# Kernel optimization log

Hardware: AMD Instinct MI355X
Metric: run time of the kernel (lower is better)

The kernel has to match this reference:

```python
import jax, jax.numpy as jnp
import numpy as np
import math

D_MODEL = 1024
H = 16
D_K = D_MODEL // H
D_FF = 4096
NEG = -1e9


def layer_norm(x, alpha, bias):
    # Faithful to source: mean over last dim, UNBIASED std (torch.std default),
    # eps defined in source but never used in forward.
    mean = jnp.mean(x, axis=-1, keepdims=True)
    std = jnp.std(x, axis=-1, ddof=1, keepdims=True)
    return (x - mean) / std * alpha + bias


def mha(x, mask, w_q, w_k, w_v, w_o):
    B, S, D = x.shape
    q = (x @ w_q.T).reshape(B, S, H, D_K)
    k = (x @ w_k.T).reshape(B, S, H, D_K)
    v = (x @ w_v.T).reshape(B, S, H, D_K)
    scores = jnp.einsum('bqhd,bkhd->bhqk', q, k) / math.sqrt(D_K)
    scores = jnp.where(mask, NEG, scores)
    attn = jax.nn.softmax(scores, axis=-1)
    out = jnp.einsum('bhqk,bkhd->bqhd', attn, v).reshape(B, S, D)
    return out @ w_o.T


def setup_inputs() -> dict:
    key = jax.random.key(0)
    ks = jax.random.split(key, 16)
    B, S = 4, 2048
    s = 0.02
    return {
        'x': jax.random.normal(ks[0], (B, S, D_MODEL), jnp.float32),
        'w_q': jax.random.normal(ks[1], (D_MODEL, D_MODEL), jnp.float32) * s,
        'w_k': jax.random.normal(ks[2], (D_MODEL, D_MODEL), jnp.float32) * s,
        'w_v': jax.random.normal(ks[3], (D_MODEL, D_MODEL), jnp.float32) * s,
        'w_o': jax.random.normal(ks[4], (D_MODEL, D_MODEL), jnp.float32) * s,
        'l1_w': jax.random.normal(ks[5], (D_FF, D_MODEL), jnp.float32) * s,
        'l1_b': jnp.zeros((D_FF,), jnp.float32),
        'l2_w': jax.random.normal(ks[6], (D_MODEL, D_FF), jnp.float32) * s,
        'l2_b': jnp.zeros((D_MODEL,), jnp.float32),
        'norm1_a': jnp.ones((D_MODEL,), jnp.float32),
        'norm1_b': jnp.zeros((D_MODEL,), jnp.float32),
        'norm2_a': jnp.ones((D_MODEL,), jnp.float32),
        'norm2_b': jnp.zeros((D_MODEL,), jnp.float32),
        'normf_a': jnp.ones((D_MODEL,), jnp.float32),
        'normf_b': jnp.zeros((D_MODEL,), jnp.float32),
        'mask': jax.random.randint(ks[7], (B, 1, 1, S), 0, 2) == 1,
    }


def reference(x, w_q, w_k, w_v, w_o, l1_w, l1_b, l2_w, l2_b,
              norm1_a, norm1_b, norm2_a, norm2_b, normf_a, normf_b, mask):
    # residual 1: pre-norm self-attention (dropout is identity at eval)
    x = x + mha(layer_norm(x, norm1_a, norm1_b), mask, w_q, w_k, w_v, w_o)
    # residual 2: pre-norm FFN
    h = layer_norm(x, norm2_a, norm2_b)
    ff = jax.nn.relu(h @ l1_w.T + l1_b) @ l2_w.T + l2_b
    x = x + ff
    return layer_norm(x, normf_a, normf_b)
```

## Files before the change

kernel.cpp:

```cpp
#include <hip/hip_runtime.h>
#include <hip/hip_bf16.h>


typedef __bf16 bf16x8 __attribute__((ext_vector_type(8)));
typedef float f32x4 __attribute__((ext_vector_type(4)));
typedef unsigned short u16x8 __attribute__((ext_vector_type(8)));
using bf16 = __hip_bfloat16;

__device__ __forceinline__ f32x4 mfma16(bf16x8 a, bf16x8 b, f32x4 c) {
  return __builtin_amdgcn_mfma_f32_16x16x32_bf16(a, b, c, 0, 0, 0);
}

__device__ __forceinline__ int swz(int row, int blk) {
  return row * 64 + ((blk ^ (row & 7)) << 3);
}

__device__ __forceinline__ void stage_tile64(unsigned short* lds,
                                             const bf16* g, int ld, int rows) {
  const int lane = threadIdx.x & 63, wid = threadIdx.x >> 6;
  const int r8 = lane >> 3, blk = lane & 7;
  const bf16* gl = g + (size_t)r8 * ld + ((blk ^ r8) << 3);
  const int passes = rows >> 3;
  for (int p = wid; p < passes; p += 4) {
    __builtin_amdgcn_global_load_lds(
        (const __attribute__((address_space(1))) void*)(gl + (size_t)(p * 8) * ld),
        (__attribute__((address_space(3))) void*)(lds + p * 512),
        16, 0, 0);
  }
}

__device__ __forceinline__ short bfb(float x) {
  return (short)__hip_bfloat16_raw(__float2bfloat16(x)).x;
}

__global__ __launch_bounds__(256) void cvt_k(const float* __restrict__ s,
                                             bf16* __restrict__ d, int n) {
  const int i = (blockIdx.x * 256 + threadIdx.x) * 4;
  if (i + 3 < n) {
    const float4 v = *reinterpret_cast<const float4*>(s + i);
    ushort4 o;
    o.x = (unsigned short)bfb(v.x);
    o.y = (unsigned short)bfb(v.y);
    o.z = (unsigned short)bfb(v.z);
    o.w = (unsigned short)bfb(v.w);
    *reinterpret_cast<ushort4*>(d + i) = o;
  }
}

template <bool OUT_F32>
__global__ __launch_bounds__(256) void layernorm_k(const float* __restrict__ in,
                                                   const float* __restrict__ gamma,
                                                   const float* __restrict__ beta,
                                                   void* __restrict__ out) {
  __shared__ float red[8];
  const int row = blockIdx.x, t = threadIdx.x;
  const float4 vv = reinterpret_cast<const float4*>(in + (size_t)row * 1024)[t];
  const float x0 = vv.x, x1 = vv.y, x2 = vv.z, x3 = vv.w;
  float s = x0 + x1 + x2 + x3;
#pragma unroll
  for (int off = 32; off; off >>= 1) s += __shfl_down(s, off);
  if ((t & 63) == 0) red[t >> 6] = s;
  __syncthreads();
  const float mean = (red[0] + red[1] + red[2] + red[3]) * (1.0f / 1024.0f);
  const float d0 = x0 - mean, d1 = x1 - mean, d2 = x2 - mean, d3 = x3 - mean;
  float sq = d0 * d0 + d1 * d1 + d2 * d2 + d3 * d3;
#pragma unroll
  for (int off = 32; off; off >>= 1) sq += __shfl_down(sq, off);
  if ((t & 63) == 0) red[4 + (t >> 6)] = sq;
  __syncthreads();
  const float var =
      fmaxf((red[4] + red[5] + red[6] + red[7]) * (1.0f / 1023.0f), 1e-20f);
  const float rstd = rsqrtf(var);
  const float4 ga = reinterpret_cast<const float4*>(gamma)[t];
  const float4 be = reinterpret_cast<const float4*>(beta)[t];
  const float y0 = d0 * rstd * ga.x + be.x;
  const float y1 = d1 * rstd * ga.y + be.y;
  const float y2 = d2 * rstd * ga.z + be.z;
  const float y3 = d3 * rstd * ga.w + be.w;
  if (OUT_F32) {
    reinterpret_cast<float4*>((float*)out + (size_t)row * 1024)[t] =
        make_float4(y0, y1, y2, y3);
  } else {
    ushort4 o;
    o.x = (unsigned short)bfb(y0);
    o.y = (unsigned short)bfb(y1);
    o.z = (unsigned short)bfb(y2);
    o.w = (unsigned short)bfb(y3);
    reinterpret_cast<ushort4*>((bf16*)out + (size_t)row * 1024)[t] = o;
  }
}

template <bool HAS_BIAS, bool RELU, bool HAS_RES, bool OUT_F32>
__global__ __launch_bounds__(256) void gemm_bt(const bf16* __restrict__ A,
                                               const bf16* __restrict__ W,
                                               const float* __restrict__ bias,
                                               const float* __restrict__ resid,
                                               void* __restrict__ out,
                                               int M, int N, int K,
                                               int lda, int ldw) {
  __shared__ __align__(16) unsigned short As[128 * 64];
  __shared__ __align__(16) unsigned short Bs[128 * 64];
  const int lane = threadIdx.x & 63, wid = threadIdx.x >> 6;
  const int n16 = lane & 15, quad = lane >> 4;
  const int wm = (wid >> 1) * 64, wn = (wid & 1) * 64;
  const int tm = blockIdx.x * 128, tn = blockIdx.y * 128;
  f32x4 acc[4][4] = {};
  for (int k0 = 0; k0 < K; k0 += 64) {
    stage_tile64(As, A + (size_t)tm * lda + k0, lda, 128);
    stage_tile64(Bs, W + (size_t)tn * ldw + k0, ldw, 128);
    __syncthreads();
#pragma unroll
    for (int kk = 0; kk < 64; kk += 32) {
      bf16x8 af[4], bw[4];
#pragma unroll
      for (int i = 0; i < 4; ++i)
        af[i] = *reinterpret_cast<const bf16x8*>(
            &As[swz(wm + i * 16 + n16, (kk >> 3) + quad)]);
#pragma unroll
      for (int j = 0; j < 4; ++j)
        bw[j] = *reinterpret_cast<const bf16x8*>(
            &Bs[swz(wn + j * 16 + n16, (kk >> 3) + quad)]);
#pragma unroll
      for (int i = 0; i < 4; ++i)
#pragma unroll
        for (int j = 0; j < 4; ++j) acc[i][j] = mfma16(af[i], bw[j], acc[i][j]);
    }
    __syncthreads();
  }
#pragma unroll
  for (int i = 0; i < 4; ++i) {
#pragma unroll
    for (int j = 0; j < 4; ++j) {
      const int n = tn + wn + j * 16 + n16;
      const float bv = HAS_BIAS ? bias[n] : 0.0f;
#pragma unroll
      for (int r = 0; r < 4; ++r) {
        const int m = tm + wm + i * 16 + quad * 4 + r;
        float vv = acc[i][j][r] + bv;
        if (RELU) vv = fmaxf(vv, 0.0f);
        if (HAS_RES) vv += resid[(size_t)m * N + n];
        if (OUT_F32)
          ((float*)out)[(size_t)m * N + n] = vv;
        else
          ((bf16*)out)[(size_t)m * N + n] = __float2bfloat16(vv);
      }
    }
  }
}

__global__ __launch_bounds__(256) void gemm_qkv_k(const bf16* __restrict__ ln1,
                                                  const bf16* __restrict__ cln,
                                                  const bf16* __restrict__ wqkv,
                                                  const int* __restrict__ cnt,
                                                  bf16* __restrict__ qout,
                                                  bf16* __restrict__ kvout) {
  __shared__ __align__(16) unsigned short As[128 * 64];
  __shared__ __align__(16) unsigned short Bs[128 * 64];
  const int tm = blockIdx.x * 128, by = blockIdx.y;
  const bool isQ = (by < 8);
  if (!isQ) {
    const int npad = (cnt[tm >> 11] + 127) & ~127;
    if ((tm & 2047) >= npad) return;
  }
  const bf16* Ap = isQ ? ln1 : cln;
  const int tn = by * 128;
  const int lane = threadIdx.x & 63, wid = threadIdx.x >> 6;
  const int n16 = lane & 15, quad = lane >> 4;
  const int wm = (wid >> 1) * 64, wn = (wid & 1) * 64;
  f32x4 acc[4][4] = {};
  for (int k0 = 0; k0 < 1024; k0 += 64) {
    stage_tile64(As, Ap + (size_t)tm * 1024 + k0, 1024, 128);
    stage_tile64(Bs, wqkv + (size_t)tn * 1024 + k0, 1024, 128);
    __syncthreads();
#pragma unroll
    for (int kk = 0; kk < 64; kk += 32) {
      bf16x8 af[4], bw[4];
#pragma unroll
      for (int i = 0; i < 4; ++i)
        af[i] = *reinterpret_cast<const bf16x8*>(
            &As[swz(wm + i * 16 + n16, (kk >> 3) + quad)]);
#pragma unroll
      for (int j = 0; j < 4; ++j)
        bw[j] = *reinterpret_cast<const bf16x8*>(
            &Bs[swz(wn + j * 16 + n16, (kk >> 3) + quad)]);
#pragma unroll
      for (int i = 0; i < 4; ++i)
#pragma unroll
        for (int j = 0; j < 4; ++j) acc[i][j] = mfma16(af[i], bw[j], acc[i][j]);
    }
    __syncthreads();
  }
  bf16* outp = isQ ? qout : kvout;
  const int ldo = isQ ? 1024 : 2048;
  const int nc0 = isQ ? tn : tn - 1024;
#pragma unroll
  for (int i = 0; i < 4; ++i) {
#pragma unroll
    for (int j = 0; j < 4; ++j) {
      const int n = nc0 + wn + j * 16 + n16;
#pragma unroll
      for (int r = 0; r < 4; ++r) {
        const int m = tm + wm + i * 16 + quad * 4 + r;
        outp[(size_t)m * ldo + n] = __float2bfloat16(acc[i][j][r]);
      }
    }
  }
}

__global__ __launch_bounds__(256) void prep_mask_k(const int* __restrict__ m,
                                                   float* __restrict__ mf,
                                                   int n) {
  __shared__ int s;
  if (threadIdx.x == 0) s = 0;
  __syncthreads();
  unsigned int acc = 0;
  for (int i = threadIdx.x; i < 512; i += 256)
    acc |= ((const unsigned int*)m)[i] & 0xFFFFFF00u;
  if (acc) atomicOr(&s, 1);
  __syncthreads();
  const bool bytes = (s != 0);
  const int i = blockIdx.x * 256 + threadIdx.x;
  if (i < n) {
    const int v = bytes ? (int)((const unsigned char*)m)[i] : m[i];
    mf[i] = v ? -1.4427e9f : 0.0f;
  }
}

__global__ __launch_bounds__(256) void scan_k(const float* __restrict__ maskf,
                                              float* __restrict__ cmask,
                                              int* __restrict__ idx,
                                              int* __restrict__ cnt) {
  __shared__ int wsum[4];
  const int b = blockIdx.x, t = threadIdx.x, lane = t & 63, w = t >> 6;
  const float* mrow = maskf + b * 2048;
  int keep[8], local = 0;
#pragma unroll
  for (int e = 0; e < 8; ++e) {
    keep[e] = (mrow[t * 8 + e] == 0.0f) ? 1 : 0;
    local += keep[e];
  }
  int inc = local;
#pragma unroll
  for (int off = 1; off < 64; off <<= 1) {
    int v = __shfl_up(inc, off);
    if (lane >= off) inc += v;
  }
  if (lane == 63) wsum[w] = inc;
  __syncthreads();
  int base = 0;
#pragma unroll
  for (int i = 0; i < 4; ++i)
    if (i < w) base += wsum[i];
  int p = base + inc - local;
#pragma unroll
  for (int e = 0; e < 8; ++e)
    if (keep[e]) idx[b * 2048 + p++] = t * 8 + e;
  const int total = wsum[0] + wsum[1] + wsum[2] + wsum[3];
  if (t == 0) cnt[b] = total;
  for (int i = t; i < 2048; i += 256)
    cmask[b * 2048 + i] = (i < total) ? 0.0f : -1.4427e9f;
}

__global__ __launch_bounds__(128) void gatherA_k(const bf16* __restrict__ ln1,
                                                 const int* __restrict__ idx,
                                                 const int* __restrict__ cnt,
                                                 bf16* __restrict__ cln) {
  const int b = blockIdx.x >> 11, j = blockIdx.x & 2047;
  const int n = cnt[b];
  const int npad = (n + 127) & ~127;
  if (j >= npad) return;
  u16x8* dst = reinterpret_cast<u16x8*>(cln + ((size_t)(b * 2048 + j)) * 1024);
  if (j < n) {
    const int s = idx[b * 2048 + j];
    const u16x8* src =
        reinterpret_cast<const u16x8*>(ln1 + ((size_t)(b * 2048 + s)) * 1024);
    dst[threadIdx.x] = src[threadIdx.x];
  } else {
    u16x8 z = {};
    dst[threadIdx.x] = z;
  }
}

__global__ __launch_bounds__(256) void attn_k(const bf16* __restrict__ q,
                                              const bf16* __restrict__ kv,
                                              const float* __restrict__ cmask,
                                              const int* __restrict__ cnt,
                                              bf16* __restrict__ out, int BHN) {
  __shared__ __align__(16) unsigned short Ks[2][64 * 64];
  __shared__ __align__(16) unsigned short Vs[2][64 * 72];
  const int lane = threadIdx.x & 63, wid = threadIdx.x >> 6;
  const int n16 = lane & 15, quad = lane >> 4;
  const int bid = blockIdx.x;
  const int bh = bid % BHN, qb = bid / BHN;
  const int b = bh >> 4, h = bh & 15;
  const bf16* qp0 = q + (size_t)b * 2048 * 1024 + h * 64;
  const bf16* kp0 = kv + (size_t)b * 2048 * 2048 + h * 64;
  const bf16* vp0 = kp0 + 1024;
  const float* mfb = cmask + b * 2048;
  const int cntb = cnt[b];
  const int nk = ((cntb + 63) >> 6) << 6;
  const int qrow0 = qb * 128 + wid * 32;

  bf16x8 qf[2][2];
#pragma unroll
  for (int g = 0; g < 2; ++g) {
    const bf16* qp = qp0 + (size_t)(qrow0 + g * 16 + n16) * 1024 + quad * 8;
    qf[g][0] = *reinterpret_cast<const bf16x8*>(qp);
    qf[g][1] = *reinterpret_cast<const bf16x8*>(qp + 32);
  }
  bf16x8 ones;
#pragma unroll
  for (int e = 0; e < 8; ++e) ones[e] = (__bf16)1.0f;
  f32x4 oacc[2][4] = {};
  f32x4 lacc[2] = {};
  const int prow = ((n16 >> 2) << 3) + (n16 & 3);
  const int vkey = lane, vdc = wid * 16;

  stage_tile64(Ks[0], kp0, 2048, 64);
  {
    const bf16* vp = vp0 + (size_t)vkey * 2048 + vdc;
    const u16x8 a = *reinterpret_cast<const u16x8*>(vp);
    const u16x8 bq = *reinterpret_cast<const u16x8*>(vp + 8);
#pragma unroll
    for (int e = 0; e < 8; ++e) {
      Vs[0][(vdc + e) * 72 + vkey] = a[e];
      Vs[0][(vdc + 8 + e) * 72 + vkey] = bq[e];
    }
  }
  int cur = 0;
  for (int kt = 0; kt < nk; kt += 64) {
    __syncthreads();
    const bool hasNext = (kt + 64 < nk);
    const bool fullTile = (kt + 64 <= cntb);
    u16x8 na = {}, nb = {};
    if (hasNext) {
      stage_tile64(Ks[cur ^ 1], kp0 + (size_t)(kt + 64) * 2048, 2048, 64);
      const bf16* vp = vp0 + (size_t)(kt + 64 + vkey) * 2048 + vdc;
      na = *reinterpret_cast<const u16x8*>(vp);
      nb = *reinterpret_cast<const u16x8*>(vp + 8);
    }
    const unsigned short* Kc = Ks[cur];
    const unsigned short* Vc = Vs[cur];
#pragma unroll
    for (int sub = 0; sub < 2; ++sub) {
      const int kb = sub * 32;
      bf16x8 aflo[2], afhi[2];
#pragma unroll
      for (int st = 0; st < 2; ++st) {
        const int row = kb + prow + st * 4;
        aflo[st] = *reinterpret_cast<const bf16x8*>(&Kc[swz(row, quad)]);
        afhi[st] = *reinterpret_cast<const bf16x8*>(&Kc[swz(row, 4 + quad)]);
      }
      __builtin_amdgcn_s_setprio(1);
      f32x4 z[2][2];
#pragma unroll
      for (int g = 0; g < 2; ++g)
#pragma unroll
        for (int st = 0; st < 2; ++st) {
          f32x4 zz = {};
          zz = mfma16(aflo[st], qf[g][0], zz);
          zz = mfma16(afhi[st], qf[g][1], zz);
          z[g][st] = zz;
        }
      __builtin_amdgcn_s_setprio(0);
      float4 m0 = make_float4(0.f, 0.f, 0.f, 0.f);
      float4 m1 = make_float4(0.f, 0.f, 0.f, 0.f);
      if (!fullTile) {
        m0 = *reinterpret_cast<const float4*>(mfb + kt + kb + quad * 8);
        m1 = *reinterpret_cast<const float4*>(mfb + kt + kb + quad * 8 + 4);
      }
      bf16x8 vf[4];
#pragma unroll
      for (int j = 0; j < 4; ++j)
        vf[j] = *reinterpret_cast<const bf16x8*>(
            &Vc[(j * 16 + n16) * 72 + kb + quad * 8]);
#pragma unroll
      for (int g = 0; g < 2; ++g) {
        bf16x8 pf;
#pragma unroll
        for (int r = 0; r < 4; ++r) {
          const float e0 = __builtin_amdgcn_exp2f(
              fmaf(z[g][0][r], 0.18033688f, ((const float*)&m0)[r]));
          const float e1 = __builtin_amdgcn_exp2f(
              fmaf(z[g][1][r], 0.18033688f, ((const float*)&m1)[r]));
          pf[r] = (__bf16)e0;
          pf[4 + r] = (__bf16)e1;
        }
        __builtin_amdgcn_s_setprio(1);
#pragma unroll
        for (int j = 0; j < 4; ++j) oacc[g][j] = mfma16(pf, vf[j], oacc[g][j]);
        lacc[g] = mfma16(pf, ones, lacc[g]);
        __builtin_amdgcn_s_setprio(0);
      }
    }
    if (hasNext) {
      unsigned short* Vn = Vs[cur ^ 1];
#pragma unroll
      for (int e = 0; e < 8; ++e) {
        Vn[(vdc + e) * 72 + vkey] = na[e];
        Vn[(vdc + 8 + e) * 72 + vkey] = nb[e];
      }
    }
    cur ^= 1;
  }
#pragma unroll
  for (int g = 0; g < 2; ++g) {
#pragma unroll
    for (int r = 0; r < 4; ++r) {
      const float lr = 1.0f / fmaxf(lacc[g][r], 1e-20f);
      bf16* op =
          out + (size_t)(b * 2048 + qrow0 + g * 16 + quad * 4 + r) * 1024 +
          h * 64;
#pragma unroll
      for (int j = 0; j < 4; ++j)
        op[j * 16 + n16] = __float2bfloat16(oacc[g][j][r] * lr);
    }
  }
}

extern "C" void kernel_launch(void* const* d_in, const int* in_sizes, int n_in,
                              void* d_out, int out_size, void* d_ws,
                              size_t ws_size, hipStream_t stream) {
  const float* x    = (const float*)d_in[0];
  const float* w_q  = (const float*)d_in[1];
  const float* w_k  = (const float*)d_in[2];
  const float* w_v  = (const float*)d_in[3];
  const float* w_o  = (const float*)d_in[4];
  const float* l1_w = (const float*)d_in[5];
  const float* l1_b = (const float*)d_in[6];
  const float* l2_w = (const float*)d_in[7];
  const float* l2_b = (const float*)d_in[8];
  const float* n1a  = (const float*)d_in[9];
  const float* n1b  = (const float*)d_in[10];
  const float* n2a  = (const float*)d_in[11];
  const float* n2b  = (const float*)d_in[12];
  const float* nfa  = (const float*)d_in[13];
  const float* nfb  = (const float*)d_in[14];
  const int* mask   = (const int*)d_in[15];

  const int D = 1024, FF = 4096;
  const int M = in_sizes[0] / D;
  const int B = M / 2048;

  const size_t MB = 1024ull * 1024ull;
  if (ws_size < 121 * MB) return;
  char* w = (char*)d_ws;
  bf16* WQKV = (bf16*)(w + 0 * MB);
  bf16* WO   = (bf16*)(w + 6 * MB);
  bf16* L1W  = (bf16*)(w + 8 * MB);
  bf16* L2W  = (bf16*)(w + 16 * MB);
  bf16* LN1  = (bf16*)(w + 24 * MB);
  bf16* Qbuf = (bf16*)(w + 40 * MB);
  bf16* ATT  = LN1;
  bf16* HLN  = (bf16*)(w + 40 * MB);
  bf16* CLN  = (bf16*)(w + 56 * MB);
  bf16* FF1  = (bf16*)(w + 56 * MB);
  bf16* KV   = (bf16*)(w + 88 * MB);
  float* X1  = (float*)(w + 88 * MB);
  float* MASKF = (float*)(w + 120 * MB);
  float* CMASK = (float*)(w + 120 * MB + 256 * 1024);
  int*   IDX   = (int*)(w + 120 * MB + 512 * 1024);
  int*   CNT   = (int*)(w + 120 * MB + 768 * 1024);

  const dim3 blk(256);
  cvt_k<<<dim3(D * D / 1024), blk, 0, stream>>>(w_q, WQKV, D * D);
  cvt_k<<<dim3(D * D / 1024), blk, 0, stream>>>(w_k, WQKV + D * D, D * D);
  cvt_k<<<dim3(D * D / 1024), blk, 0, stream>>>(w_v, WQKV + 2 * D * D, D * D);
  cvt_k<<<dim3(D * D / 1024), blk, 0, stream>>>(w_o, WO, D * D);
  cvt_k<<<dim3(FF * D / 1024), blk, 0, stream>>>(l1_w, L1W, FF * D);
  cvt_k<<<dim3(FF * D / 1024), blk, 0, stream>>>(l2_w, L2W, FF * D);
  prep_mask_k<<<dim3((M + 255) / 256), blk, 0, stream>>>(mask, MASKF, M);
  scan_k<<<dim3(B), blk, 0, stream>>>(MASKF, CMASK, IDX, CNT);

  layernorm_k<false><<<M, blk, 0, stream>>>(x, n1a, n1b, LN1);
  gatherA_k<<<dim3(B * 2048), dim3(128), 0, stream>>>(LN1, IDX, CNT, CLN);
  gemm_qkv_k<<<dim3(M / 128, 24), blk, 0, stream>>>(LN1, CLN, WQKV, CNT, Qbuf,
                                                    KV);
  const int BHN = B * 16;
  attn_k<<<dim3((M / 128) * 16), blk, 0, stream>>>(Qbuf, KV, CMASK, CNT, ATT,
                                                   BHN);
  gemm_bt<false, false, true, true><<<dim3(M / 128, D / 128), blk, 0, stream>>>(
      ATT, WO, nullptr, x, X1, M, D, D, D, D);
  layernorm_k<false><<<M, blk, 0, stream>>>(X1, n2a, n2b, HLN);
  for (int c = 0; c < 2; ++c) {
    gemm_bt<true, true, false, false>
        <<<dim3(M / 128, 2048 / 128), blk, 0, stream>>>(
            HLN, L1W + (size_t)c * 2048 * D, l1_b + c * 2048, nullptr, FF1, M,
            2048, D, D, D);
    if (c == 0)
      gemm_bt<true, false, true, true>
          <<<dim3(M / 128, D / 128), blk, 0, stream>>>(
              FF1, L2W + c * 2048, l2_b, X1, X1, M, D, 2048, 2048, FF);
    else
      gemm_bt<false, false, true, true>
          <<<dim3(M / 128, D / 128), blk, 0, stream>>>(
              FF1, L2W + c * 2048, nullptr, X1, X1, M, D, 2048, 2048, FF);
  }
  layernorm_k<true><<<M, blk, 0, stream>>>(X1, nfa, nfb, (float*)d_out);
}
```

Measured before the change: 518.0 us.

## Replace QKV and FF1 GEMMs with 256x256 double-buffered 512-thread kernel

```diff
diff --git a/kernel.cpp b/kernel.cpp
--- a/kernel.cpp
+++ b/kernel.cpp
@@ -27,6 +27,19 @@
         (__attribute__((address_space(3))) void*)(lds + p * 512),
         16, 0, 0);
   }
+}
+
+__device__ __forceinline__ void stage_half512(unsigned short* lds,
+                                              const bf16* g, int ld) {
+  const int lane = threadIdx.x & 63, w8 = threadIdx.x >> 6;
+  const int r8 = lane >> 3, blk = lane & 7;
+  const bf16* gl = g + (size_t)r8 * ld + ((blk ^ r8) << 3);
+  __builtin_amdgcn_global_load_lds(
+      (const __attribute__((address_space(1))) void*)(gl + (size_t)(w8 * 8) * ld),
+      (__attribute__((address_space(3))) void*)(lds + w8 * 512), 16, 0, 0);
+  __builtin_amdgcn_global_load_lds(
+      (const __attribute__((address_space(1))) void*)(gl + (size_t)((w8 + 8) * 8) * ld),
+      (__attribute__((address_space(3))) void*)(lds + (w8 + 8) * 512), 16, 0, 0);
 }
 
 __device__ __forceinline__ short bfb(float x) {
@@ -148,60 +161,114 @@
   }
 }
 
-__global__ __launch_bounds__(256) void gemm_qkv_k(const bf16* __restrict__ ln1,
-                                                  const bf16* __restrict__ cln,
-                                                  const bf16* __restrict__ wqkv,
-                                                  const int* __restrict__ cnt,
-                                                  bf16* __restrict__ qout,
-                                                  bf16* __restrict__ kvout) {
-  __shared__ __align__(16) unsigned short As[128 * 64];
-  __shared__ __align__(16) unsigned short Bs[128 * 64];
-  const int tm = blockIdx.x * 128, by = blockIdx.y;
-  const bool isQ = (by < 8);
-  if (!isQ) {
-    const int npad = (cnt[tm >> 11] + 127) & ~127;
-    if ((tm & 2047) >= npad) return;
-  }
-  const bf16* Ap = isQ ? ln1 : cln;
-  const int tn = by * 128;
-  const int lane = threadIdx.x & 63, wid = threadIdx.x >> 6;
+template <bool QKV, bool HAS_BIAS, bool RELU>
+__global__ __launch_bounds__(512, 2) void gemm256_k(
+    const bf16* __restrict__ A0, const bf16* __restrict__ cln,
+    const bf16* __restrict__ W, const float* __restrict__ bias,
+    const int* __restrict__ cnt, bf16* __restrict__ out,
+    bf16* __restrict__ kvout, int M, int N, int K, int lda, int ldw) {
+  __shared__ __align__(16) unsigned short Lds[65536];
+  const int tm = blockIdx.x * 256;
+  const int tn = blockIdx.y * 256;
+  const bf16* A = A0;
+  bool isQ = true;
+  if (QKV) {
+    isQ = (blockIdx.y < 4);
+    if (!isQ) {
+      const int npad = (cnt[tm >> 11] + 127) & ~127;
+      if ((tm & 2047) >= npad) return;
+      A = cln;
+    }
+  }
+  const int lane = threadIdx.x & 63, w8 = threadIdx.x >> 6;
   const int n16 = lane & 15, quad = lane >> 4;
-  const int wm = (wid >> 1) * 64, wn = (wid & 1) * 64;
-  f32x4 acc[4][4] = {};
-  for (int k0 = 0; k0 < 1024; k0 += 64) {
-    stage_tile64(As, Ap + (size_t)tm * 1024 + k0, 1024, 128);
-    stage_tile64(Bs, wqkv + (size_t)tn * 1024 + k0, 1024, 128);
-    __syncthreads();
-#pragma unroll
-    for (int kk = 0; kk < 64; kk += 32) {
-      bf16x8 af[4], bw[4];
-#pragma unroll
-      for (int i = 0; i < 4; ++i)
-        af[i] = *reinterpret_cast<const bf16x8*>(
-            &As[swz(wm + i * 16 + n16, (kk >> 3) + quad)]);
-#pragma unroll
-      for (int j = 0; j < 4; ++j)
-        bw[j] = *reinterpret_cast<const bf16x8*>(
-            &Bs[swz(wn + j * 16 + n16, (kk >> 3) + quad)]);
-#pragma unroll
-      for (int i = 0; i < 4; ++i)
-#pragma unroll
-        for (int j = 0; j < 4; ++j) acc[i][j] = mfma16(af[i], bw[j], acc[i][j]);
-    }
-    __syncthreads();
-  }
-  bf16* outp = isQ ? qout : kvout;
-  const int ldo = isQ ? 1024 : 2048;
-  const int nc0 = isQ ? tn : tn - 1024;
-#pragma unroll
-  for (int i = 0; i < 4; ++i) {
+  const int wm = (w8 >> 2) << 7;
+  const int wn = (w8 & 3) << 6;
+  const int NT = K >> 6;
+  const unsigned short* LAb = Lds + ((wm >> 7) * 8192);
+  const unsigned short* LBb = Lds + 16384 + ((wn >> 7) * 8192);
+  const int browB = wn & 127;
+  f32x4 acc[8][4] = {};
+#pragma unroll
+  for (int pt = 0; pt < 2; ++pt) {
+    unsigned short* base = Lds + pt * 32768;
+    const bf16* Ag = A + (size_t)tm * lda + pt * 64;
+    const bf16* Wg = W + (size_t)tn * ldw + pt * 64;
+    stage_half512(base, Ag, lda);
+    stage_half512(base + 8192, Ag + (size_t)128 * lda, lda);
+    stage_half512(base + 16384, Wg, ldw);
+    stage_half512(base + 24576, Wg + (size_t)128 * ldw, ldw);
+  }
+  for (int t = 0; t < NT; ++t) {
+    const int bofs = (t & 1) * 32768;
+    if (t + 1 < NT)
+      asm volatile("s_waitcnt vmcnt(8)" ::: "memory");
+    else
+      asm volatile("s_waitcnt vmcnt(0)" ::: "memory");
+    __builtin_amdgcn_sched_barrier(0);
+    __builtin_amdgcn_s_barrier();
+    const unsigned short* LA = LAb + bofs;
+    const unsigned short* LB = LBb + bofs;
+    bf16x8 bfr[4][2];
+#pragma unroll
+    for (int j = 0; j < 4; ++j) {
+      const int br = browB + j * 16 + n16;
+      bfr[j][0] = *reinterpret_cast<const bf16x8*>(&LB[swz(br, quad)]);
+      bfr[j][1] = *reinterpret_cast<const bf16x8*>(&LB[swz(br, 4 + quad)]);
+    }
+#pragma unroll
+    for (int ph = 0; ph < 4; ++ph) {
+      bf16x8 af0[2], af1[2];
+#pragma unroll
+      for (int ii = 0; ii < 2; ++ii) {
+        const int ar = (ph * 2 + ii) * 16 + n16;
+        af0[ii] = *reinterpret_cast<const bf16x8*>(&LA[swz(ar, quad)]);
+        af1[ii] = *reinterpret_cast<const bf16x8*>(&LA[swz(ar, 4 + quad)]);
+      }
+      __builtin_amdgcn_s_setprio(1);
+#pragma unroll
+      for (int ii = 0; ii < 2; ++ii)
+#pragma unroll
+        for (int j = 0; j < 4; ++j) {
+          f32x4 c = acc[ph * 2 + ii][j];
+          c = mfma16(af0[ii], bfr[j][0], c);
+          c = mfma16(af1[ii], bfr[j][1], c);
+          acc[ph * 2 + ii][j] = c;
+        }
+      __builtin_amdgcn_s_setprio(0);
+      __builtin_amdgcn_s_barrier();
+    }
+    if (t + 2 < NT) {
+      unsigned short* base = Lds + bofs;
+      const bf16* Ag = A + (size_t)tm * lda + (t + 2) * 64;
+      const bf16* Wg = W + (size_t)tn * ldw + (t + 2) * 64;
+      stage_half512(base, Ag, lda);
+      stage_half512(base + 8192, Ag + (size_t)128 * lda, lda);
+      stage_half512(base + 16384, Wg, ldw);
+      stage_half512(base + 24576, Wg + (size_t)128 * ldw, ldw);
+    }
+  }
+  bf16* op;
+  int ldo, nc0;
+  if (QKV && !isQ) {
+    op = kvout; ldo = 2048; nc0 = tn - 1024;
+  } else if (QKV) {
+    op = out; ldo = 1024; nc0 = tn;
+  } else {
+    op = out; ldo = N; nc0 = tn;
+  }
+#pragma unroll
+  for (int i = 0; i < 8; ++i) {
 #pragma unroll
     for (int j = 0; j < 4; ++j) {
       const int n = nc0 + wn + j * 16 + n16;
+      const float bv = HAS_BIAS ? bias[n] : 0.0f;
 #pragma unroll
       for (int r = 0; r < 4; ++r) {
         const int m = tm + wm + i * 16 + quad * 4 + r;
-        outp[(size_t)m * ldo + n] = __float2bfloat16(acc[i][j][r]);
+        float vv = acc[i][j][r] + bv;
+        if (RELU) vv = fmaxf(vv, 0.0f);
+        op[(size_t)m * ldo + n] = __float2bfloat16(vv);
       }
     }
   }
@@ -474,8 +541,8 @@
 
   layernorm_k<false><<<M, blk, 0, stream>>>(x, n1a, n1b, LN1);
   gatherA_k<<<dim3(B * 2048), dim3(128), 0, stream>>>(LN1, IDX, CNT, CLN);
-  gemm_qkv_k<<<dim3(M / 128, 24), blk, 0, stream>>>(LN1, CLN, WQKV, CNT, Qbuf,
-                                                    KV);
+  gemm256_k<true, false, false><<<dim3(M / 256, 12), dim3(512), 0, stream>>>(
+      LN1, CLN, WQKV, nullptr, CNT, Qbuf, KV, M, 3072, 1024, 1024, 1024);
   const int BHN = B * 16;
   attn_k<<<dim3((M / 128) * 16), blk, 0, stream>>>(Qbuf, KV, CMASK, CNT, ATT,
                                                    BHN);
@@ -483,10 +550,9 @@
       ATT, WO, nullptr, x, X1, M, D, D, D, D);
   layernorm_k<false><<<M, blk, 0, stream>>>(X1, n2a, n2b, HLN);
   for (int c = 0; c < 2; ++c) {
-    gemm_bt<true, true, false, false>
-        <<<dim3(M / 128, 2048 / 128), blk, 0, stream>>>(
-            HLN, L1W + (size_t)c * 2048 * D, l1_b + c * 2048, nullptr, FF1, M,
-            2048, D, D, D);
+    gemm256_k<false, true, true><<<dim3(M / 256, 8), dim3(512), 0, stream>>>(
+        HLN, nullptr, L1W + (size_t)c * 2048 * D, l1_b + c * 2048, nullptr,
+        FF1, nullptr, M, 2048, 1024, 1024, 1024);
     if (c == 0)
       gemm_bt<true, false, true, true>
           <<<dim3(M / 128, D / 128), blk, 0, stream>>>(
```

Result: no change. 516.6 us (-0.3%).
